# Kernel optimization log

Measured on AMD Instinct MI355X. Metric: run time of the kernel, lower is better.

## Reference

```python
import jax, jax.numpy as jnp
import numpy as np

B, EVI, L, H, K, NL = 16, 5, 128, 768, 21, 3
SIGMA = 0.1

def _kernel_mus(n):
    mu = [1.0]
    bin_size = 2.0 / (n - 1)
    mu.append(1 - bin_size / 2)
    for i in range(1, n - 1):
        mu.append(mu[i] - bin_size)
    return mu

MU = np.asarray(_kernel_mus(K), dtype=np.float32)                      # [K]
SIG = np.asarray([0.001] + [SIGMA] * (K - 1), dtype=np.float32)        # [K]


def setup_inputs() -> dict:
    key = jax.random.key(0)
    ks = jax.random.split(key, 8)
    std = 0.02
    inputs_hiddens = jax.random.normal(ks[0], (B, EVI, L, H), jnp.float32)
    inputs = jax.random.normal(ks[1], (B, EVI, H), jnp.float32)
    # mask_text: valid tokens with CLS (position 0) zeroed, as in torch forward
    mask_text = jnp.ones((B, EVI, L), jnp.float32).at[:, :, 0].set(0.0)
    seg = (jnp.arange(L) >= L // 2).astype(jnp.float32)  # first half = claim, second = evidence
    mask_claim = (1.0 - seg) * mask_text
    mask_evidence = seg * mask_text
    return {
        "inputs_hiddens": inputs_hiddens,
        "inputs": inputs,
        "mask_text": mask_text,
        "mask_claim": mask_claim,
        "mask_evidence": mask_evidence,
        "W_att": jax.random.normal(ks[2], (K, 1), jnp.float32) * std,
        "b_att": jnp.zeros((1,), jnp.float32),
        "W_sel": jax.random.normal(ks[3], (K, 1), jnp.float32) * std,
        "b_sel": jnp.zeros((1,), jnp.float32),
        "gat_W1": jax.random.normal(ks[4], (2 * H, 128), jnp.float32) * std,
        "gat_b1": jnp.zeros((128,), jnp.float32),
        "gat_W2": jax.random.normal(ks[5], (128, 1), jnp.float32) * std,
        "gat_b2": jnp.zeros((1,), jnp.float32),
        "inf_W": jax.random.normal(ks[6], (2 * H, NL), jnp.float32) * std,
        "inf_b": jnp.zeros((NL,), jnp.float32),
    }


def _l2norm(x):
    # F.normalize(p=2, dim=-1) with eps=1e-12
    return x / jnp.maximum(jnp.linalg.norm(x, axis=-1, keepdims=True), 1e-12)


def _kernel_pool(sim, attn_d):
    # sim: [N, Lq, Ld]; attn_d: [N, Ld]  ->  [N, Lq, K]
    # exp(-(sim - mu)^2 / (2 sigma^2)) masked by doc attention, summed over doc tokens
    pv = jnp.exp(-((sim[..., None] - MU) ** 2) / (2.0 * SIG ** 2)) * attn_d[:, None, :, None]
    return pv.sum(axis=2)


def _intersect_att(qn, dn, attn_q, attn_d, W_att, b_att):
    # token-level attention scores over q tokens: [N, Lq]
    sim = jnp.einsum('nqh,ndh->nqd', qn, dn)
    lp = jnp.log(jnp.maximum(_kernel_pool(sim, attn_d), 1e-10))  # [N, Lq, K]
    lp = (lp @ W_att + b_att)[..., 0]                            # [N, Lq]
    lp = jnp.where(attn_q == 0.0, -1e4, lp)
    return jax.nn.softmax(lp, axis=1)


def _intersect_sel(qn, dn, attn_q, attn_d, W_sel, b_sel):
    # per-pair evidence selection logit: [N, 1]
    sim = jnp.einsum('nqh,ndh->nqd', qn, dn)
    lp = jnp.log(jnp.maximum(_kernel_pool(sim, attn_d), 1e-10)) * attn_q[..., None] * 0.01
    lp = lp.sum(axis=1) / (attn_q.sum(axis=1, keepdims=True) + 1e-10)  # [N, K]
    return lp @ W_sel + b_sel


def _gat(x, W1, b1, W2, b2):
    # proj_gat: Linear(2H,128) -> ReLU -> Linear(128,1)
    return jnp.maximum(x @ W1 + b1, 0.0) @ W2 + b2


def reference(inputs_hiddens, inputs, mask_text, mask_claim, mask_evidence,
              W_att, b_att, W_sel, b_sel, gat_W1, gat_b1, gat_W2, gat_b2,
              inf_W, inf_b):
    hid = inputs_hiddens                          # [B, EVI, L, H]
    hn = _l2norm(hid)
    hn_flat = hn.reshape(-1, L, H)

    # evidence selection prior over EVI pieces
    sel = _intersect_sel(hn_flat, hn_flat,
                         mask_claim.reshape(-1, L), mask_evidence.reshape(-1, L),
                         W_sel, b_sel)
    select_prob = jax.nn.softmax(sel.reshape(B, EVI, 1), axis=1)

    att_de = []
    for i in range(EVI):  # fixed small structural loop
        own_n = hn[:, i]                           # [B, L, H]
        own_mask = mask_text[:, i]                 # [B, L]
        dn = jnp.broadcast_to(own_n[:, None], (B, EVI, L, H)).reshape(-1, L, H)
        dm = jnp.broadcast_to(own_mask[:, None], (B, EVI, L)).reshape(-1, L)
        att = _intersect_att(hn_flat, dn, mask_evidence.reshape(-1, L), dm, W_att, b_att)
        att = att.reshape(B, EVI, L, 1)
        denoise = (att * hid).sum(axis=2)          # [B, EVI, H]
        own_inp = jnp.broadcast_to(inputs[:, i:i + 1], (B, EVI, H))
        w_de = jax.nn.softmax(_gat(jnp.concatenate([own_inp, denoise], -1),
                                   gat_W1, gat_b1, gat_W2, gat_b2), axis=1)  # [B, EVI, 1]
        att_de.append((denoise * w_de).sum(axis=1))  # [B, H]

    att_de = jnp.stack(att_de, axis=1)             # [B, EVI, H]
    feats = jnp.concatenate([inputs, att_de], axis=-1)  # [B, EVI, 2H]
    class_prob = jax.nn.softmax(feats @ inf_W + inf_b, axis=2)
    prob = jnp.log((select_prob * class_prob).sum(axis=1))  # [B, NL]
    return prob
```

## Files before the change

kernel.cpp:

```cpp
#include <hip/hip_runtime.h>
#include <math.h>

#define NB 16
#define NE 5
#define LL 128
#define HH 768
#define NK 21
#define NCLS 3
#define NN (NB*NE)

typedef float f32x4 __attribute__((ext_vector_type(4)));
typedef float f32x8 __attribute__((ext_vector_type(8)));
typedef short s16x8 __attribute__((ext_vector_type(8)));

__device__ __forceinline__ short bf16rne(float f) {
    union { float f; unsigned u; } c; c.f = f;
    unsigned u = c.u;
    unsigned r = (u + 0x7FFFu + ((u >> 16) & 1u)) >> 16;
    return (short)r;
}
__device__ __forceinline__ float sum8(f32x8 x) {
    return ((x[0] + x[1]) + (x[2] + x[3])) + ((x[4] + x[5]) + (x[6] + x[7]));
}
__device__ __forceinline__ f32x8 exp2v(f32x8 x) {
    f32x8 r;
    r[0] = exp2f(x[0]); r[1] = exp2f(x[1]); r[2] = exp2f(x[2]); r[3] = exp2f(x[3]);
    r[4] = exp2f(x[4]); r[5] = exp2f(x[5]); r[6] = exp2f(x[6]); r[7] = exp2f(x[7]);
    return r;
}
__device__ __forceinline__ f32x8 mk8(float4 a, float4 b) {
    f32x8 r;
    r[0] = a.x; r[1] = a.y; r[2] = a.z; r[3] = a.w;
    r[4] = b.x; r[5] = b.y; r[6] = b.z; r[7] = b.w;
    return r;
}
__device__ __forceinline__ float dot4(float4 a, float4 b) {
    return fmaf(a.x, b.x, fmaf(a.y, b.y, fmaf(a.z, b.z, a.w * b.w)));
}

__global__ __launch_bounds__(256) void k_prep(const float* __restrict__ hid,
                                              short* __restrict__ hswz,
                                              const float* __restrict__ W1,
                                              float* __restrict__ w1t) {
    __shared__ float sT[64][65];
    const int tid = threadIdx.x;
    if (blockIdx.x >= 640) {
        const int bb = blockIdx.x - 640;
        const int tI = bb >> 1, jI = bb & 1;
        #pragma unroll
        for (int i = 0; i < 16; ++i) {
            const int r = (tid >> 6) + i * 4, c = tid & 63;
            sT[r][c] = W1[(size_t)(tI * 64 + r) * 128 + jI * 64 + c];
        }
        __syncthreads();
        #pragma unroll
        for (int i = 0; i < 16; ++i) {
            const int r = (tid >> 6) + i * 4, c = tid & 63;
            w1t[(size_t)(jI * 64 + r) * 1536 + tI * 64 + c] = sT[c][r];
        }
        return;
    }
    const int n = blockIdx.x >> 3, slab = blockIdx.x & 7;
    const int l = tid & 63, w = tid >> 6;
    float* sInv = &sT[0][0];
    #pragma unroll
    for (int rr = 0; rr < 4; ++rr) {
        const int lr = w * 4 + rr;
        const int row = slab * 16 + lr;
        const float4* rp = reinterpret_cast<const float4*>(hid + ((size_t)n * LL + row) * HH);
        float4 a = rp[l], b = rp[l + 64], c = rp[l + 128];
        float ss = a.x*a.x + a.y*a.y + a.z*a.z + a.w*a.w
                 + b.x*b.x + b.y*b.y + b.z*b.z + b.w*b.w
                 + c.x*c.x + c.y*c.y + c.z*c.z + c.w*c.w;
        #pragma unroll
        for (int o = 32; o > 0; o >>= 1) ss += __shfl_xor(ss, o, 64);
        if (l == 0) sInv[lr] = 1.0f / fmaxf(sqrtf(ss), 1e-12f);
    }
    __syncthreads();
    const float* base = hid + (size_t)n * LL * HH;
    s16x8* dst = reinterpret_cast<s16x8*>(hswz) + (size_t)n * 12288;
    #pragma unroll
    for (int i = 0; i < 6; ++i) {
        const int uid = i * 256 + tid;
        const int s = uid >> 6, sub = uid & 63;
        const int r15 = sub >> 2, kc = sub & 3;
        const int row = slab * 16 + r15;
        const int k0 = s * 32 + kc * 8;
        const float4* p = reinterpret_cast<const float4*>(base + (size_t)row * HH + k0);
        float4 v0 = p[0], v1 = p[1];
        const float inv = sInv[r15];
        s16x8 h;
        h[0] = bf16rne(v0.x * inv); h[1] = bf16rne(v0.y * inv);
        h[2] = bf16rne(v0.z * inv); h[3] = bf16rne(v0.w * inv);
        h[4] = bf16rne(v1.x * inv); h[5] = bf16rne(v1.y * inv);
        h[6] = bf16rne(v1.z * inv); h[7] = bf16rne(v1.w * inv);
        dst[(size_t)s * 512 + slab * 64 + kc * 16 + r15] = h;
    }
}

__global__ __launch_bounds__(256, 2) void k_simpool(
    const short* __restrict__ hswz,
    const float* __restrict__ mask_text, const float* __restrict__ mask_claim,
    const float* __restrict__ mask_evidence,
    const float* __restrict__ W_att, const float* __restrict__ b_att,
    const float* __restrict__ W_sel,
    float* __restrict__ attw, float2* __restrict__ dselPart)
{
    const int bid = blockIdx.x;
    const int b = bid & 15, rest = bid >> 4;
    const int pair = rest >> 1, qh = rest & 1;
    const int e = pair / NE, ep = pair - e * NE;
    const int nq = b * NE + e, nd = b * NE + ep;
    const bool diag = (e == ep);
    const int tid = threadIdx.x, lane = tid & 63, w = tid >> 6;
    const int lx = lane & 15, lg = lane >> 4;

    __shared__ s16x8 sB[2][1024];
    __shared__ __align__(16) float sMT[LL];
    __shared__ __align__(16) float sMEd[LL];
    __shared__ float sMEq[64], sMCq[64], sSel[64];
    __shared__ float sWA[NK], sWS[NK], sCK[NK];

    if (tid < 128) {
        sMT[tid]  = mask_text[nd * LL + tid];
        sMEd[tid] = mask_evidence[nd * LL + tid];
    } else if (tid < 192) {
        const int q = tid - 128;
        sMEq[q] = mask_evidence[nq * LL + qh * 64 + q];
        sMCq[q] = mask_claim[nq * LL + qh * 64 + q];
    } else if (tid < 192 + NK) {
        sWA[tid - 192] = W_att[tid - 192] * 0.69314718f;
    } else if (tid < 213 + NK) {
        sWS[tid - 213] = W_sel[tid - 213] * 0.69314718f;
    } else if (tid < 254) {
        const int k = tid - 233;
        const float kk = (float)(k - 1);
        sCK[k] = exp2f(fmaf(kk, 13.7056029f, fmaf(kk * kk, -0.72134752f, -32.0f)));
    } else if (tid == 254) {
        sCK[0] = 1.0f;
    }

    const s16x8* gA = reinterpret_cast<const s16x8*>(hswz) + (size_t)nq * 12288;
    const s16x8* gB = reinterpret_cast<const s16x8*>(hswz) + (size_t)nd * 12288;

    sB[0][tid] = gB[tid];
    sB[0][tid + 256] = gB[tid + 256];
    sB[0][tid + 512] = gB[tid + 512];
    sB[0][tid + 768] = gB[tid + 768];
    const int arow = (qh * 4 + w) * 64 + lane;
    s16x8 aC0 = gA[arow];
    s16x8 aC1 = gA[512 + arow];

    f32x4 acc[8];
    #pragma unroll
    for (int nj = 0; nj < 8; ++nj) acc[nj] = (f32x4){0.f, 0.f, 0.f, 0.f};

    __syncthreads();

    for (int s = 0; s < 12; ++s) {
        const int cur = s & 1;
        s16x8 nB0, nB1, nB2, nB3, aN0, aN1;
        if (s < 11) {
            const s16x8* gBs = gB + (s + 1) * 1024;
            nB0 = gBs[tid]; nB1 = gBs[tid + 256];
            nB2 = gBs[tid + 512]; nB3 = gBs[tid + 768];
            aN0 = gA[(s + 1) * 1024 + arow];
            aN1 = gA[(s + 1) * 1024 + 512 + arow];
        }
        #pragma unroll
        for (int nj = 0; nj < 8; ++nj)
            acc[nj] = __builtin_amdgcn_mfma_f32_16x16x32_bf16(aC0, sB[cur][nj * 64 + lane], acc[nj], 0, 0, 0);
        #pragma unroll
        for (int nj = 0; nj < 8; ++nj)
            acc[nj] = __builtin_amdgcn_mfma_f32_16x16x32_bf16(aC1, sB[cur][512 + nj * 64 + lane], acc[nj], 0, 0, 0);
        if (s < 11) {
            sB[1 - cur][tid] = nB0; sB[1 - cur][tid + 256] = nB1;
            sB[1 - cur][tid + 512] = nB2; sB[1 - cur][tid + 768] = nB3;
            aC0 = aN0; aC1 = aN1;
            __syncthreads();
        }
    }

    __syncthreads();
    float* sS = reinterpret_cast<float*>(sB);
    {
        const int rxw0 = w * 16 + lg * 4;
        #pragma unroll
        for (int nj = 0; nj < 8; ++nj) {
            const int col = nj * 16 + lx;
            const int uu = col >> 2, ce = col & 3;
            #pragma unroll
            for (int r = 0; r < 4; ++r) {
                const int row = rxw0 + r;
                sS[row * 128 + ((uu ^ (row & 31)) << 2) + ce] = acc[nj][r];
            }
        }
    }
    __syncthreads();

    const int row = w * 16 + (lane & 15);
    const int sl  = lane >> 4;
    const int rx  = row & 31;
    const float4* rp = reinterpret_cast<const float4*>(sS + row * 128);

    float pk[NK], vk[NK];
    #pragma unroll
    for (int k = 0; k < NK; ++k) { pk[k] = 0.f; vk[k] = 0.f; }

    #pragma unroll
    for (int c = 0; c < 4; ++c) {
        const float4 va = rp[(sl * 8 + c * 2) ^ rx];
        const float4 vb = rp[(sl * 8 + c * 2 + 1) ^ rx];
        const f32x8 s = mk8(va, vb);
        const int j0 = sl * 32 + c * 8;
        const f32x8 m = mk8(*reinterpret_cast<const float4*>(&sMT[j0]),
                            *reinterpret_cast<const float4*>(&sMT[j0 + 4]));
        f32x8 d = s - 1.0f;
        const f32x8 g = exp2v(d * d * -721347.52f);
        pk[0] += sum8(m * g);
        const f32x8 t = exp2v(s * -14.4269504f);
        d = s - 0.95f;
        const f32x8 P = exp2v(d * d * -72.134752f + 32.0f);
        f32x8 u = m * P;
        pk[1] += sum8(u);
        #pragma unroll
        for (int k = 2; k <= 20; ++k) { u *= t; pk[k] += sum8(u); }
        if (diag) {
            const f32x8 me = mk8(*reinterpret_cast<const float4*>(&sMEd[j0]),
                                 *reinterpret_cast<const float4*>(&sMEd[j0 + 4]));
            f32x8 uv = me * P;
            vk[0] += sum8(me * g);
            vk[1] += sum8(uv);
            #pragma unroll
            for (int k = 2; k <= 20; ++k) { uv *= t; vk[k] += sum8(uv); }
        }
    }
    #pragma unroll
    for (int k = 0; k < NK; ++k) {
        pk[k] += __shfl_xor(pk[k], 16, 64);
        pk[k] += __shfl_xor(pk[k], 32, 64);
    }
    if (diag) {
        #pragma unroll
        for (int k = 0; k < NK; ++k) {
            vk[k] += __shfl_xor(vk[k], 16, 64);
            vk[k] += __shfl_xor(vk[k], 32, 64);
        }
    }
    const float bAtt = b_att[0];
    float lgt = bAtt;
    #pragma unroll
    for (int k = 0; k < NK; ++k)
        lgt = fmaf(sWA[k], log2f(fmaxf(pk[k] * sCK[k], 1e-10f)), lgt);
    if (sl == 0) {
        const size_t obase = ((size_t)ep * NN + nq) * LL + qh * 64;
        attw[obase + row] = (sMEq[row] == 0.0f) ? -10000.0f : lgt;
    }
    if (diag) {
        float rv = 0.f;
        #pragma unroll
        for (int k = 0; k < NK; ++k)
            rv = fmaf(sWS[k], log2f(fmaxf(vk[k] * sCK[k], 1e-10f)), rv);
        if (sl == 0) sSel[row] = sMCq[row] * rv;
        __syncthreads();
        if (tid < 64) {
            float su = sSel[tid], ms = sMCq[tid];
            #pragma unroll
            for (int o = 32; o > 0; o >>= 1) {
                su += __shfl_xor(su, o, 64);
                ms += __shfl_xor(ms, o, 64);
            }
            if (tid == 0) dselPart[nq * 2 + qh] = make_float2(su, ms);
        }
    }
}

__global__ __launch_bounds__(256) void k_denoise(
    const float* __restrict__ hid, const float* __restrict__ attw,
    float* __restrict__ denoi)
{
    const int blk = blockIdx.x;
    const int nq = blk / 3, ch = blk - nq * 3;
    const int tid = threadIdx.x, l = tid & 63, w = tid >> 6;
    __shared__ float sA[NE][LL];
    for (int ep = w; ep < NE; ep += 4) {
        const float* ap = attw + ((size_t)ep * NN + nq) * LL;
        float a0 = ap[l], a1 = ap[l + 64];
        float m = fmaxf(a0, a1);
        #pragma unroll
        for (int o = 32; o > 0; o >>= 1) m = fmaxf(m, __shfl_xor(m, o, 64));
        float e0 = __expf(a0 - m), e1 = __expf(a1 - m);
        float s = e0 + e1;
        #pragma unroll
        for (int o = 32; o > 0; o >>= 1) s += __shfl_xor(s, o, 64);
        float inv = 1.0f / s;
        sA[ep][l] = e0 * inv;
        sA[ep][l + 64] = e1 * inv;
    }
    __syncthreads();
    const int h = ch * 256 + tid;
    const float* hp = hid + (size_t)nq * LL * HH + h;
    float a0 = 0.f, a1 = 0.f, a2 = 0.f, a3 = 0.f, a4 = 0.f;
    #pragma unroll 8
    for (int q = 0; q < LL; ++q) {
        float x = hp[(size_t)q * HH];
        a0 = fmaf(sA[0][q], x, a0);
        a1 = fmaf(sA[1][q], x, a1);
        a2 = fmaf(sA[2][q], x, a2);
        a3 = fmaf(sA[3][q], x, a3);
        a4 = fmaf(sA[4][q], x, a4);
    }
    denoi[((size_t)0 * NN + nq) * HH + h] = a0;
    denoi[((size_t)1 * NN + nq) * HH + h] = a1;
    denoi[((size_t)2 * NN + nq) * HH + h] = a2;
    denoi[((size_t)3 * NN + nq) * HH + h] = a3;
    denoi[((size_t)4 * NN + nq) * HH + h] = a4;
}

__global__ __launch_bounds__(256) void k_gat2(
    const float* __restrict__ inputs, const float* __restrict__ denoise,
    const float* __restrict__ w1t, const float* __restrict__ b1,
    const float* __restrict__ W2, float* __restrict__ part)
{
    const int wid = blockIdx.x * 4 + (threadIdx.x >> 6);
    const int l = threadIdx.x & 63;
    const int jp = wid & 63;
    const int po = wid >> 6;
    const int j0 = jp * 2, j1 = j0 + 1;
    const int pb = po * 8;

    const float4* wc0 = reinterpret_cast<const float4*>(w1t + (size_t)j0 * 1536) + l;
    const float4* wc1 = reinterpret_cast<const float4*>(w1t + (size_t)j1 * 1536) + l;
    const float4* fin[8]; const float4* fde[8];
    #pragma unroll
    for (int u = 0; u < 8; ++u) {
        const int p = pb + u;
        const int i = p / NN; const int n2 = p - i * NN; const int bb = n2 / NE;
        fin[u] = reinterpret_cast<const float4*>(inputs + ((size_t)bb * NE + i) * HH) + l;
        fde[u] = reinterpret_cast<const float4*>(denoise + (size_t)p * HH) + l;
    }
    float a0[8], a1[8];
    #pragma unroll
    for (int u = 0; u < 8; ++u) { a0[u] = 0.f; a1[u] = 0.f; }

    #pragma unroll
    for (int it = 0; it < 3; ++it) {
        const float4 w0v = wc0[it * 64], w1v = wc1[it * 64];
        #pragma unroll
        for (int u = 0; u < 8; ++u) {
            const float4 f = fin[u][it * 64];
            a0[u] += dot4(f, w0v);
            a1[u] += dot4(f, w1v);
        }
    }
    #pragma unroll
    for (int it = 0; it < 3; ++it) {
        const float4 w0v = wc0[192 + it * 64], w1v = wc1[192 + it * 64];
        #pragma unroll
        for (int u = 0; u < 8; ++u) {
            const float4 f = fde[u][it * 64];
            a0[u] += dot4(f, w0v);
            a1[u] += dot4(f, w1v);
        }
    }
    #pragma unroll
    for (int u = 0; u < 8; ++u) {
        #pragma unroll
        for (int o = 32; o > 0; o >>= 1) {
            a0[u] += __shfl_xor(a0[u], o, 64);
            a1[u] += __shfl_xor(a1[u], o, 64);
        }
    }
    const float bb0 = b1[j0], bb1 = b1[j1], w20 = W2[j0], w21 = W2[j1];
    if (l == 0) {
        #pragma unroll
        for (int u = 0; u < 8; ++u) {
            float v = fmaxf(a0[u] + bb0, 0.f) * w20 + fmaxf(a1[u] + bb1, 0.f) * w21;
            part[(size_t)(pb + u) * 64 + jp] = v;
        }
    }
}

__global__ __launch_bounds__(256) void k_logits(
    const float* __restrict__ inputs, const float* __restrict__ denoise,
    const float* __restrict__ part, const float* __restrict__ inf_W,
    const float* __restrict__ inf_b, float* __restrict__ logi)
{
    const int bid = blockIdx.x;
    const int b = bid / NE, i = bid - b * NE;
    const int tid = threadIdx.x, l = tid & 63, wv = tid >> 6;
    __shared__ float sG[NE];
    for (int e2 = wv; e2 < NE; e2 += 4) {
        float v = part[(size_t)(i * NN + b * NE + e2) * 64 + l];
        #pragma unroll
        for (int o = 32; o > 0; o >>= 1) v += __shfl_xor(v, o, 64);
        if (l == 0) sG[e2] = v;
    }
    __syncthreads();
    float g0 = sG[0], g1 = sG[1], g2 = sG[2], g3 = sG[3], g4 = sG[4];
    float mm = fmaxf(fmaxf(fmaxf(g0, g1), fmaxf(g2, g3)), g4);
    float w0 = __expf(g0 - mm), w1 = __expf(g1 - mm), w2 = __expf(g2 - mm);
    float w3 = __expf(g3 - mm), w4 = __expf(g4 - mm);
    float inv = 1.0f / (w0 + w1 + w2 + w3 + w4);
    w0 *= inv; w1 *= inv; w2 *= inv; w3 *= inv; w4 *= inv;

    float p0 = 0.f, p1 = 0.f, p2 = 0.f;
    const float* xin = inputs + ((size_t)b * NE + i) * HH;
    const float* de = denoise + ((size_t)i * NN + b * NE) * HH;
    #pragma unroll
    for (int it = 0; it < 3; ++it) {
        int t = it * 256 + tid;
        float f = xin[t];
        p0 += f * inf_W[t * 3]; p1 += f * inf_W[t * 3 + 1]; p2 += f * inf_W[t * 3 + 2];
    }
    #pragma unroll
    for (int it = 0; it < 3; ++it) {
        int h = it * 256 + tid;
        float a = w0 * de[h] + w1 * de[HH + h] + w2 * de[2 * HH + h]
                + w3 * de[3 * HH + h] + w4 * de[4 * HH + h];
        int t = HH + h;
        p0 += a * inf_W[t * 3]; p1 += a * inf_W[t * 3 + 1]; p2 += a * inf_W[t * 3 + 2];
    }
    #pragma unroll
    for (int o = 32; o > 0; o >>= 1) {
        p0 += __shfl_xor(p0, o, 64);
        p1 += __shfl_xor(p1, o, 64);
        p2 += __shfl_xor(p2, o, 64);
    }
    __shared__ float red[4][NCLS];
    if (l == 0) { red[wv][0] = p0; red[wv][1] = p1; red[wv][2] = p2; }
    __syncthreads();
    if (tid < NCLS) {
        logi[bid * NCLS + tid] = red[0][tid] + red[1][tid] + red[2][tid] + red[3][tid]
                               + inf_b[tid];
    }
}

__global__ __launch_bounds__(64) void k_combine(
    const float2* __restrict__ dselPart, const float* __restrict__ b_sel,
    const float* __restrict__ logi, float* __restrict__ out)
{
    const int b = threadIdx.x;
    if (b >= NB) return;
    const float bs = b_sel[0];
    float d0, d1, d2, d3, d4;
#define DSEL(I, D) { float2 pa = dselPart[(b * NE + (I)) * 2], pb = dselPart[(b * NE + (I)) * 2 + 1]; \
                     (D) = bs + 0.01f * (pa.x + pb.x) / ((pa.y + pb.y) + 1e-10f); }
    DSEL(0, d0) DSEL(1, d1) DSEL(2, d2) DSEL(3, d3) DSEL(4, d4)
#undef DSEL
    float m = fmaxf(fmaxf(fmaxf(d0, d1), fmaxf(d2, d3)), d4);
    float s0 = __expf(d0 - m), s1 = __expf(d1 - m), s2 = __expf(d2 - m);
    float s3 = __expf(d3 - m), s4 = __expf(d4 - m);
    float sinv = 1.0f / (s0 + s1 + s2 + s3 + s4);
    float sp0 = s0 * sinv, sp1 = s1 * sinv, sp2 = s2 * sinv, sp3 = s3 * sinv, sp4 = s4 * sinv;
    float acc0 = 0.f, acc1 = 0.f, acc2 = 0.f;
#define CMB(I, SP) { \
        float l0 = logi[(b * NE + (I)) * NCLS], l1 = logi[(b * NE + (I)) * NCLS + 1], \
              l2 = logi[(b * NE + (I)) * NCLS + 2]; \
        float mm = fmaxf(fmaxf(l0, l1), l2); \
        float e0 = __expf(l0 - mm), e1 = __expf(l1 - mm), e2 = __expf(l2 - mm); \
        float si = 1.0f / (e0 + e1 + e2); \
        acc0 += (SP) * e0 * si; acc1 += (SP) * e1 * si; acc2 += (SP) * e2 * si; }
    CMB(0, sp0) CMB(1, sp1) CMB(2, sp2) CMB(3, sp3) CMB(4, sp4)
#undef CMB
    out[b * NCLS + 0] = logf(acc0);
    out[b * NCLS + 1] = logf(acc1);
    out[b * NCLS + 2] = logf(acc2);
}

extern "C" void kernel_launch(void* const* d_in, const int* in_sizes, int n_in,
                              void* d_out, int out_size, void* d_ws, size_t ws_size,
                              hipStream_t stream) {
    (void)in_sizes; (void)n_in; (void)out_size; (void)ws_size;
    const float* hid           = (const float*)d_in[0];
    const float* inputs        = (const float*)d_in[1];
    const float* mask_text     = (const float*)d_in[2];
    const float* mask_claim    = (const float*)d_in[3];
    const float* mask_evidence = (const float*)d_in[4];
    const float* W_att  = (const float*)d_in[5];
    const float* b_att  = (const float*)d_in[6];
    const float* W_sel  = (const float*)d_in[7];
    const float* b_sel  = (const float*)d_in[8];
    const float* gat_W1 = (const float*)d_in[9];
    const float* gat_b1 = (const float*)d_in[10];
    const float* gat_W2 = (const float*)d_in[11];
    const float* gat_b2 = (const float*)d_in[12];
    const float* inf_W  = (const float*)d_in[13];
    const float* inf_b  = (const float*)d_in[14];
    (void)gat_b2;

    short* hswz  = (short*)d_ws;
    float* denoi = (float*)((char*)d_ws + 15728640);
    float* attw  = denoi + 307200;
    float2* dselPart = (float2*)(attw + 51200);
    float* w1t   = (float*)(dselPart + 160);
    float* part  = w1t + 196608;
    float* logi  = part + 25600;

    k_prep<<<688, 256, 0, stream>>>(hid, hswz, gat_W1, w1t);
    k_simpool<<<800, 256, 0, stream>>>(hswz, mask_text, mask_claim, mask_evidence,
                                       W_att, b_att, W_sel, attw, dselPart);
    k_denoise<<<NN * 3, 256, 0, stream>>>(hid, attw, denoi);
    k_gat2<<<800, 256, 0, stream>>>(inputs, denoi, w1t, gat_b1, gat_W2, part);
    k_logits<<<NN, 256, 0, stream>>>(inputs, denoi, part, inf_W, inf_b, logi);
    k_combine<<<1, 64, 0, stream>>>(dselPart, b_sel, logi, (float*)d_out);
}
```

Baseline: 84.23 us.

## Single-buffer B tile with register prefetch and two-phase pooling to raise occupancy

Replaces the double-buffered 32KB LDS B tile with a single 16KB buffer, prefetching the next stage into registers two steps ahead, and raises launch bounds to three blocks per CU. The similarity-pooling epilogue now runs in two phases over half the rows each, reusing the smaller LDS buffer, with 8 lanes per row instead of 4. The aim is more resident blocks to hide latency, at the cost of an extra barrier per k-step and more register pressure under the tighter launch bound.

```diff
diff --git a/kernel.cpp b/kernel.cpp
--- a/kernel.cpp
+++ b/kernel.cpp
@@ -98,7 +98,7 @@
     }
 }
 
-__global__ __launch_bounds__(256, 2) void k_simpool(
+__global__ __launch_bounds__(256, 3) void k_simpool(
     const short* __restrict__ hswz,
     const float* __restrict__ mask_text, const float* __restrict__ mask_claim,
     const float* __restrict__ mask_evidence,
@@ -115,7 +115,7 @@
     const int tid = threadIdx.x, lane = tid & 63, w = tid >> 6;
     const int lx = lane & 15, lg = lane >> 4;
 
-    __shared__ s16x8 sB[2][1024];
+    __shared__ s16x8 sB[1024];
     __shared__ __align__(16) float sMT[LL];
     __shared__ __align__(16) float sMEd[LL];
     __shared__ float sMEq[64], sMCq[64], sSel[64];
@@ -143,125 +143,132 @@
     const s16x8* gA = reinterpret_cast<const s16x8*>(hswz) + (size_t)nq * 12288;
     const s16x8* gB = reinterpret_cast<const s16x8*>(hswz) + (size_t)nd * 12288;
 
-    sB[0][tid] = gB[tid];
-    sB[0][tid + 256] = gB[tid + 256];
-    sB[0][tid + 512] = gB[tid + 512];
-    sB[0][tid + 768] = gB[tid + 768];
+    {
+        s16x8 p0 = gB[tid], p1 = gB[tid + 256], p2 = gB[tid + 512], p3 = gB[tid + 768];
+        sB[tid] = p0; sB[tid + 256] = p1; sB[tid + 512] = p2; sB[tid + 768] = p3;
+    }
+    s16x8 b0 = gB[1024 + tid], b1 = gB[1024 + tid + 256],
+          b2 = gB[1024 + tid + 512], b3 = gB[1024 + tid + 768];
     const int arow = (qh * 4 + w) * 64 + lane;
     s16x8 aC0 = gA[arow];
     s16x8 aC1 = gA[512 + arow];
+    s16x8 aN0 = gA[1024 + arow];
+    s16x8 aN1 = gA[1024 + 512 + arow];
 
     f32x4 acc[8];
     #pragma unroll
     for (int nj = 0; nj < 8; ++nj) acc[nj] = (f32x4){0.f, 0.f, 0.f, 0.f};
 
-    __syncthreads();
-
     for (int s = 0; s < 12; ++s) {
-        const int cur = s & 1;
-        s16x8 nB0, nB1, nB2, nB3, aN0, aN1;
+        __syncthreads();
+        #pragma unroll
+        for (int nj = 0; nj < 8; ++nj)
+            acc[nj] = __builtin_amdgcn_mfma_f32_16x16x32_bf16(aC0, sB[nj * 64 + lane], acc[nj], 0, 0, 0);
+        #pragma unroll
+        for (int nj = 0; nj < 8; ++nj)
+            acc[nj] = __builtin_amdgcn_mfma_f32_16x16x32_bf16(aC1, sB[512 + nj * 64 + lane], acc[nj], 0, 0, 0);
         if (s < 11) {
-            const s16x8* gBs = gB + (s + 1) * 1024;
-            nB0 = gBs[tid]; nB1 = gBs[tid + 256];
-            nB2 = gBs[tid + 512]; nB3 = gBs[tid + 768];
-            aN0 = gA[(s + 1) * 1024 + arow];
-            aN1 = gA[(s + 1) * 1024 + 512 + arow];
-        }
-        #pragma unroll
-        for (int nj = 0; nj < 8; ++nj)
-            acc[nj] = __builtin_amdgcn_mfma_f32_16x16x32_bf16(aC0, sB[cur][nj * 64 + lane], acc[nj], 0, 0, 0);
-        #pragma unroll
-        for (int nj = 0; nj < 8; ++nj)
-            acc[nj] = __builtin_amdgcn_mfma_f32_16x16x32_bf16(aC1, sB[cur][512 + nj * 64 + lane], acc[nj], 0, 0, 0);
-        if (s < 11) {
-            sB[1 - cur][tid] = nB0; sB[1 - cur][tid + 256] = nB1;
-            sB[1 - cur][tid + 512] = nB2; sB[1 - cur][tid + 768] = nB3;
+            __syncthreads();
+            sB[tid] = b0; sB[tid + 256] = b1; sB[tid + 512] = b2; sB[tid + 768] = b3;
             aC0 = aN0; aC1 = aN1;
-            __syncthreads();
-        }
-    }
-
-    __syncthreads();
+            if (s < 10) {
+                const s16x8* gBs = gB + (s + 2) * 1024;
+                b0 = gBs[tid]; b1 = gBs[tid + 256];
+                b2 = gBs[tid + 512]; b3 = gBs[tid + 768];
+                aN0 = gA[(s + 2) * 1024 + arow];
+                aN1 = gA[(s + 2) * 1024 + 512 + arow];
+            }
+        }
+    }
+
     float* sS = reinterpret_cast<float*>(sB);
-    {
-        const int rxw0 = w * 16 + lg * 4;
-        #pragma unroll
-        for (int nj = 0; nj < 8; ++nj) {
-            const int col = nj * 16 + lx;
-            const int uu = col >> 2, ce = col & 3;
+    const int rloc = (w << 3) | (lane & 7);
+    const int slice = lane >> 3;
+    const int xr = lane & 7;
+    const float bAtt = b_att[0];
+    const size_t obase = ((size_t)ep * NN + nq) * LL + qh * 64;
+
+    #pragma unroll
+    for (int ph = 0; ph < 2; ++ph) {
+        __syncthreads();
+        if ((w >> 1) == ph) {
+            const int wl = w & 1;
             #pragma unroll
-            for (int r = 0; r < 4; ++r) {
-                const int row = rxw0 + r;
-                sS[row * 128 + ((uu ^ (row & 31)) << 2) + ce] = acc[nj][r];
+            for (int nj = 0; nj < 8; ++nj) {
+                const int col = nj * 16 + lx;
+                #pragma unroll
+                for (int r = 0; r < 4; ++r) {
+                    const int row = wl * 16 + lg * 4 + r;
+                    const int unit = (col >> 2) ^ (row & 7);
+                    sS[row * 128 + unit * 4 + (col & 3)] = acc[nj][r];
+                }
             }
         }
-    }
-    __syncthreads();
-
-    const int row = w * 16 + (lane & 15);
-    const int sl  = lane >> 4;
-    const int rx  = row & 31;
-    const float4* rp = reinterpret_cast<const float4*>(sS + row * 128);
-
-    float pk[NK], vk[NK];
-    #pragma unroll
-    for (int k = 0; k < NK; ++k) { pk[k] = 0.f; vk[k] = 0.f; }
-
-    #pragma unroll
-    for (int c = 0; c < 4; ++c) {
-        const float4 va = rp[(sl * 8 + c * 2) ^ rx];
-        const float4 vb = rp[(sl * 8 + c * 2 + 1) ^ rx];
-        const f32x8 s = mk8(va, vb);
-        const int j0 = sl * 32 + c * 8;
-        const f32x8 m = mk8(*reinterpret_cast<const float4*>(&sMT[j0]),
-                            *reinterpret_cast<const float4*>(&sMT[j0 + 4]));
-        f32x8 d = s - 1.0f;
-        const f32x8 g = exp2v(d * d * -721347.52f);
-        pk[0] += sum8(m * g);
-        const f32x8 t = exp2v(s * -14.4269504f);
-        d = s - 0.95f;
-        const f32x8 P = exp2v(d * d * -72.134752f + 32.0f);
-        f32x8 u = m * P;
-        pk[1] += sum8(u);
-        #pragma unroll
-        for (int k = 2; k <= 20; ++k) { u *= t; pk[k] += sum8(u); }
+        __syncthreads();
+
+        const float4* rp4 = reinterpret_cast<const float4*>(sS + rloc * 128);
+        float pk[NK], vkk[NK];
+        #pragma unroll
+        for (int k = 0; k < NK; ++k) { pk[k] = 0.f; vkk[k] = 0.f; }
+
+        #pragma unroll
+        for (int c = 0; c < 2; ++c) {
+            const float4 qa = rp4[(slice * 4 + c * 2) ^ xr];
+            const float4 qb = rp4[(slice * 4 + c * 2 + 1) ^ xr];
+            const f32x8 s = mk8(qa, qb);
+            const int j0 = slice * 16 + c * 8;
+            const f32x8 m = mk8(*reinterpret_cast<const float4*>(&sMT[j0]),
+                                *reinterpret_cast<const float4*>(&sMT[j0 + 4]));
+            f32x8 d = s - 1.0f;
+            const f32x8 g = exp2v(d * d * -721347.52f);
+            pk[0] += sum8(m * g);
+            const f32x8 t = exp2v(s * -14.4269504f);
+            d = s - 0.95f;
+            const f32x8 P = exp2v(d * d * -72.134752f + 32.0f);
+            f32x8 u = m * P;
+            pk[1] += sum8(u);
+            #pragma unroll
+            for (int k = 2; k <= 20; ++k) { u *= t; pk[k] += sum8(u); }
+            if (diag) {
+                const f32x8 me = mk8(*reinterpret_cast<const float4*>(&sMEd[j0]),
+                                     *reinterpret_cast<const float4*>(&sMEd[j0 + 4]));
+                f32x8 uv = me * P;
+                vkk[0] += sum8(me * g);
+                vkk[1] += sum8(uv);
+                #pragma unroll
+                for (int k = 2; k <= 20; ++k) { uv *= t; vkk[k] += sum8(uv); }
+            }
+        }
+        #pragma unroll
+        for (int k = 0; k < NK; ++k) {
+            pk[k] += __shfl_xor(pk[k], 8, 64);
+            pk[k] += __shfl_xor(pk[k], 16, 64);
+            pk[k] += __shfl_xor(pk[k], 32, 64);
+        }
         if (diag) {
-            const f32x8 me = mk8(*reinterpret_cast<const float4*>(&sMEd[j0]),
-                                 *reinterpret_cast<const float4*>(&sMEd[j0 + 4]));
-            f32x8 uv = me * P;
-            vk[0] += sum8(me * g);
-            vk[1] += sum8(uv);
             #pragma unroll
-            for (int k = 2; k <= 20; ++k) { uv *= t; vk[k] += sum8(uv); }
-        }
-    }
-    #pragma unroll
-    for (int k = 0; k < NK; ++k) {
-        pk[k] += __shfl_xor(pk[k], 16, 64);
-        pk[k] += __shfl_xor(pk[k], 32, 64);
+            for (int k = 0; k < NK; ++k) {
+                vkk[k] += __shfl_xor(vkk[k], 8, 64);
+                vkk[k] += __shfl_xor(vkk[k], 16, 64);
+                vkk[k] += __shfl_xor(vkk[k], 32, 64);
+            }
+        }
+        const int grow = ph * 32 + rloc;
+        float lgt = bAtt;
+        #pragma unroll
+        for (int k = 0; k < NK; ++k)
+            lgt = fmaf(sWA[k], log2f(fmaxf(pk[k] * sCK[k], 1e-10f)), lgt);
+        if (slice == 0)
+            attw[obase + grow] = (sMEq[grow] == 0.0f) ? -10000.0f : lgt;
+        if (diag) {
+            float rv = 0.f;
+            #pragma unroll
+            for (int k = 0; k < NK; ++k)
+                rv = fmaf(sWS[k], log2f(fmaxf(vkk[k] * sCK[k], 1e-10f)), rv);
+            if (slice == 0) sSel[grow] = sMCq[grow] * rv;
+        }
     }
     if (diag) {
-        #pragma unroll
-        for (int k = 0; k < NK; ++k) {
-            vk[k] += __shfl_xor(vk[k], 16, 64);
-            vk[k] += __shfl_xor(vk[k], 32, 64);
-        }
-    }
-    const float bAtt = b_att[0];
-    float lgt = bAtt;
-    #pragma unroll
-    for (int k = 0; k < NK; ++k)
-        lgt = fmaf(sWA[k], log2f(fmaxf(pk[k] * sCK[k], 1e-10f)), lgt);
-    if (sl == 0) {
-        const size_t obase = ((size_t)ep * NN + nq) * LL + qh * 64;
-        attw[obase + row] = (sMEq[row] == 0.0f) ? -10000.0f : lgt;
-    }
-    if (diag) {
-        float rv = 0.f;
-        #pragma unroll
-        for (int k = 0; k < NK; ++k)
-            rv = fmaf(sWS[k], log2f(fmaxf(vk[k] * sCK[k], 1e-10f)), rv);
-        if (sl == 0) sSel[row] = sMCq[row] * rv;
         __syncthreads();
         if (tid < 64) {
             float su = sSel[tid], ms = sMCq[tid];
```

After: 92.77 us. +10.1%, slower.
